# Kernel optimization log

Hardware: AMD Instinct MI355X
Metric: run time of the kernel (lower is better)

The kernel has to match this reference:

```python
import jax, jax.numpy as jnp
import numpy as np

N, F_IN, H, HEADS, C, E = 4096, 768, 512, 4, 32, 131072
DH = H // HEADS


def gcn_conv(x, W, b, src, dst):
    # PyG GCNConv: add self-loops, symmetric normalization, scatter-add aggregation
    h = x @ W                                   # [N, H_out]
    loop = jnp.arange(N)
    s = jnp.concatenate([src, loop])            # sources incl self-loops
    d = jnp.concatenate([dst, loop])            # targets incl self-loops
    deg = jax.ops.segment_sum(jnp.ones_like(d, dtype=h.dtype), d, num_segments=N)
    dinv = jnp.where(deg > 0, jax.lax.rsqrt(deg), 0.0)
    norm = dinv[s] * dinv[d]                    # [E+N]
    msg = h[s] * norm[:, None]                  # gather + scale
    out = jax.ops.segment_sum(msg, d, num_segments=N)  # scatter-add
    return out + b


def mha(x, in_w, in_b, out_w, out_b):
    # torch.nn.MultiheadAttention, batch=1, q=k=v=x, eval (no dropout)
    qkv = x @ in_w.T + in_b                     # [N, 3H]
    q, k, v = jnp.split(qkv, 3, axis=-1)
    q = q.reshape(N, HEADS, DH)
    k = k.reshape(N, HEADS, DH)
    v = v.reshape(N, HEADS, DH)
    scale = 1.0 / jnp.sqrt(jnp.asarray(DH, x.dtype))
    scores = jnp.einsum('nhd,mhd->hnm', q * scale, k)   # [HEADS, N, N]
    attn = jax.nn.softmax(scores, axis=-1)
    o = jnp.einsum('hnm,mhd->nhd', attn, v).reshape(N, H)
    return o @ out_w.T + out_b


def setup_inputs() -> dict:
    key = jax.random.key(0)
    ks = jax.random.split(key, 12)
    f32 = jnp.float32
    return {
        'x': jax.random.normal(ks[0], (N, F_IN), dtype=f32),
        'edge_index': jax.random.randint(ks[1], (2, E), 0, N, dtype=jnp.int64),
        'W1': jax.random.normal(ks[2], (F_IN, H), dtype=f32) * (1.0 / np.sqrt(F_IN)),
        'b1': jnp.zeros((H,), dtype=f32),
        'in_w': jax.random.normal(ks[3], (3 * H, H), dtype=f32) * (1.0 / np.sqrt(H)),
        'in_b': jnp.zeros((3 * H,), dtype=f32),
        'out_w': jax.random.normal(ks[4], (H, H), dtype=f32) * (1.0 / np.sqrt(H)),
        'out_b': jnp.zeros((H,), dtype=f32),
        'W2': jax.random.normal(ks[5], (H, H), dtype=f32) * (1.0 / np.sqrt(H)),
        'b2': jnp.zeros((H,), dtype=f32),
        'Wc': jax.random.normal(ks[6], (H, C), dtype=f32) * (1.0 / np.sqrt(H)),
        'bc': jnp.zeros((C,), dtype=f32),
    }


def reference(x, edge_index, W1, b1, in_w, in_b, out_w, out_b, W2, b2, Wc, bc):
    src, dst = edge_index[0], edge_index[1]
    h = jax.nn.relu(gcn_conv(x, W1, b1, src, dst))
    h = h + mha(h, in_w, in_b, out_w, out_b)      # residual; dropout is identity (eval)
    h = jax.nn.relu(gcn_conv(h, W2, b2, src, dst))
    return h @ Wc + bc                             # [N, C]
```

## Files before the change

kernel.cpp:

```cpp
#include <hip/hip_runtime.h>

typedef unsigned short u16;
typedef unsigned int u32;
typedef __attribute__((ext_vector_type(8))) short bf16x8;
typedef __attribute__((ext_vector_type(4))) short bf16x4;
typedef __attribute__((ext_vector_type(4))) float f32x4;
typedef __attribute__((ext_vector_type(16))) float f32x16;

__device__ __forceinline__ float b2f(u16 b){ u32 u = ((u32)b)<<16; float f; __builtin_memcpy(&f,&u,4); return f; }
__device__ __forceinline__ u16 f2b(float f){ u32 u; __builtin_memcpy(&u,&f,4); u32 r = (u + 0x7fffu + ((u>>16)&1u)) >> 16; return (u16)r; }
__device__ __forceinline__ u32 cvtpk(float lo, float hi){ u32 r; asm("v_cvt_pk_bf16_f32 %0, %1, %2" : "=v"(r) : "v"(lo), "v"(hi)); return r; }
__device__ __forceinline__ void pswap(u32 &a, u32 &b){ asm("v_permlane32_swap_b32 %0, %1" : "+v"(a), "+v"(b)); }
__device__ __forceinline__ void gload16(const u16* g, u16* l){
  __builtin_amdgcn_global_load_lds((const __attribute__((address_space(1))) void*)g,
                                   (__attribute__((address_space(3))) void*)l, 16, 0, 0);
}

__device__ __forceinline__ void conv_body(const float* __restrict__ in, u16* __restrict__ out, int b, int n){
  int i = (b*256 + threadIdx.x)*4;
  if (i + 3 < n){
    float4 v = *(const float4*)(in + i);
    bf16x4 o;
    o[0]=(short)f2b(v.x); o[1]=(short)f2b(v.y); o[2]=(short)f2b(v.z); o[3]=(short)f2b(v.w);
    *(bf16x4*)(out + i) = o;
  } else {
    for (; i<n; ++i) out[i]=f2b(in[i]);
  }
}
__global__ __launch_bounds__(256) void prep_k(const float* __restrict__ x, const float* __restrict__ inw,
    const float* __restrict__ outw, const float* __restrict__ W1, const float* __restrict__ W2,
    const float* __restrict__ Wc, const int* __restrict__ dst, int E,
    u16* __restrict__ Xb, u16* __restrict__ inWb, u16* __restrict__ outWb,
    u16* __restrict__ W1T, u16* __restrict__ W2T, u16* __restrict__ WcT, int* __restrict__ deg){
  __shared__ float tile[32][33];
  int b = blockIdx.x;
  if (b < 3072){ conv_body(x, Xb, b, 4096*768); return; }
  if (b < 3840){ conv_body(inw, inWb, b-3072, 1536*512); return; }
  if (b < 4096){ conv_body(outw, outWb, b-3840, 512*512); return; }
  if (b < 4752){
    const float* in; u16* out; int R, C, bx, by;
    if (b < 4480){ in=W1; out=W1T; R=768; C=512; int lb=b-4096; bx=lb&15; by=lb>>4; }
    else if (b < 4736){ in=W2; out=W2T; R=512; C=512; int lb=b-4480; bx=lb&15; by=lb>>4; }
    else { in=Wc; out=WcT; R=512; C=32; bx=0; by=b-4736; }
    int tx = threadIdx.x & 31, ty = threadIdx.x >> 5;
    int c0 = bx*32, r0 = by*32;
    #pragma unroll
    for (int k=0;k<4;++k){
      int r = r0 + ty + k*8, c = c0 + tx;
      if (r < R && c < C) tile[ty+k*8][tx] = in[(size_t)r*C + c];
    }
    __syncthreads();
    #pragma unroll
    for (int k=0;k<4;++k){
      int c = c0 + ty + k*8, r = r0 + tx;
      if (r < R && c < C) out[(size_t)c*R + r] = f2b(tile[tx][ty+k*8]);
    }
    return;
  }
  int e = (b-4752)*256 + threadIdx.x;
  if (e < E) atomicAdd(&deg[dst[e]], 1);
}

__global__ __launch_bounds__(256) void scan_k(const int* __restrict__ deg, int* __restrict__ row_ptr,
                                              int* __restrict__ cursor, float* __restrict__ dinv){
  __shared__ int lds[256];
  int t = threadIdx.x;
  int base = t*16;
  int cnt[16]; int s = 0;
  #pragma unroll
  for (int k=0;k<16;++k){
    int d = deg[base+k] + 1;
    cnt[k] = d - 1;
    s += d - 1;
    dinv[base+k] = 1.0f / sqrtf((float)d);
  }
  lds[t] = s; __syncthreads();
  for (int o=1;o<256;o<<=1){
    int v = (t>=o) ? lds[t-o] : 0;
    __syncthreads();
    lds[t] += v;
    __syncthreads();
  }
  int run = lds[t] - s;
  #pragma unroll
  for (int k=0;k<16;++k){ row_ptr[base+k] = run; cursor[base+k] = run; run += cnt[k]; }
  if (t == 255) row_ptr[4096] = run;
}
__global__ __launch_bounds__(256) void scatter_k(const int* __restrict__ src, const int* __restrict__ dst,
                                                 int* __restrict__ cursor, int* __restrict__ srcl, int E){
  int e = blockIdx.x*256 + threadIdx.x;
  if (e < E){
    int d = dst[e];
    int pos = atomicAdd(&cursor[d], 1);
    srcl[pos] = src[e];
  }
}

__global__ __launch_bounds__(64) void aggregate_k(const u16* __restrict__ H, const float* __restrict__ dinv,
                                                  const int* __restrict__ rp, const int* __restrict__ srcl,
                                                  const float* __restrict__ bias, u16* __restrict__ out){
  const int i = blockIdx.x, t = threadIdx.x;
  const float di = dinv[i];
  float a[8];
  {
    bf16x8 hv = *(const bf16x8*)(H + (size_t)i*512 + t*8);
    float wself = di*di;
    #pragma unroll
    for (int j=0;j<8;++j) a[j] = b2f((u16)hv[j])*wself;
  }
  int e0 = rp[i], e1 = rp[i+1];
  int e = e0;
  for (; e+3 < e1; e += 4){
    int s0 = srcl[e], s1 = srcl[e+1], s2 = srcl[e+2], s3 = srcl[e+3];
    float w0 = dinv[s0]*di, w1 = dinv[s1]*di, w2 = dinv[s2]*di, w3 = dinv[s3]*di;
    bf16x8 v0 = *(const bf16x8*)(H + (size_t)s0*512 + t*8);
    bf16x8 v1 = *(const bf16x8*)(H + (size_t)s1*512 + t*8);
    bf16x8 v2 = *(const bf16x8*)(H + (size_t)s2*512 + t*8);
    bf16x8 v3 = *(const bf16x8*)(H + (size_t)s3*512 + t*8);
    #pragma unroll
    for (int j=0;j<8;++j){
      a[j] += b2f((u16)v0[j])*w0 + b2f((u16)v1[j])*w1 + b2f((u16)v2[j])*w2 + b2f((u16)v3[j])*w3;
    }
  }
  for (; e < e1; ++e){
    int s = srcl[e];
    float w = dinv[s]*di;
    bf16x8 v = *(const bf16x8*)(H + (size_t)s*512 + t*8);
    #pragma unroll
    for (int j=0;j<8;++j) a[j] += b2f((u16)v[j])*w;
  }
  bf16x8 o;
  #pragma unroll
  for (int j=0;j<8;++j){
    float v = fmaxf(a[j] + bias[t*8+j], 0.f);
    o[j] = (short)f2b(v);
  }
  *(bf16x8*)(out + (size_t)i*512 + t*8) = o;
}

template<int BM,int BN,int WM,int WN,bool BIAS,bool RESID,bool RELU,bool OUTBF,bool QKV>
__global__ __launch_bounds__(256) void gemm_abt_k(
    const u16* __restrict__ A, const u16* __restrict__ B,
    const float* __restrict__ bias, const u16* __restrict__ resid,
    u16* __restrict__ vt, void* __restrict__ Cp, int M, int N, int K)
{
  constexpr int BK = 64;
  constexpr int AISS = (BM*BK)/(256*8);
  constexpr int BISS = (BN*BK)/(256*8);
  constexpr int WC = BN/WN;
  constexpr int FM = WM/16, FN = WN/16;
  constexpr float QS = 0.088388347648318447f * 1.4426950408889634f;
  __shared__ u16 As[BM*BK];
  __shared__ u16 Bs[BN*BK];
  const int tid = threadIdx.x;
  const int wv = tid>>6, ln = tid&63;
  const int l15 = ln&15, l4 = ln>>4;
  const int wm = wv / WC, wn = wv % WC;
  const int bm0 = blockIdx.x*BM, bn0 = blockIdx.y*BN;
  const int arow = tid>>3;
  const int acol = (tid&7)*8;
  f32x4 acc[FM][FN];
  #pragma unroll
  for (int a=0;a<FM;++a)
    #pragma unroll
    for (int b=0;b<FN;++b) acc[a][b] = f32x4{0.f,0.f,0.f,0.f};
  for (int kt=0; kt<K; kt+=BK){
    #pragma unroll
    for (int i=0;i<AISS;++i) gload16(A + (size_t)(bm0 + i*32 + arow)*K + kt + acol, &As[i*2048 + wv*512]);
    #pragma unroll
    for (int i=0;i<BISS;++i) gload16(B + (size_t)(bn0 + i*32 + arow)*K + kt + acol, &Bs[i*2048 + wv*512]);
    __syncthreads();
    #pragma unroll
    for (int kc=0;kc<2;++kc){
      bf16x8 af[FM], bfr[FN];
      #pragma unroll
      for (int a=0;a<FM;++a) af[a] = *(const bf16x8*)(&As[(wm*WM + a*16 + l15)*BK + kc*32 + l4*8]);
      #pragma unroll
      for (int b=0;b<FN;++b) bfr[b] = *(const bf16x8*)(&Bs[(wn*WN + b*16 + l15)*BK + kc*32 + l4*8]);
      #pragma unroll
      for (int a=0;a<FM;++a)
        #pragma unroll
        for (int b=0;b<FN;++b)
          acc[a][b] = __builtin_amdgcn_mfma_f32_16x16x32_bf16(af[a], bfr[b], acc[a][b], 0,0,0);
    }
    __syncthreads();
  }
  #pragma unroll
  for (int a=0;a<FM;++a)
    #pragma unroll
    for (int b=0;b<FN;++b){
      int r0 = bm0 + wm*WM + a*16 + l4*4;
      int c  = bn0 + wn*WN + b*16 + l15;
      if constexpr (QKV){
        float v0 = acc[a][b][0] + bias[c];
        float v1 = acc[a][b][1] + bias[c];
        float v2 = acc[a][b][2] + bias[c];
        float v3 = acc[a][b][3] + bias[c];
        if (c >= 1024){
          bf16x4 pk; pk[0]=(short)f2b(v0); pk[1]=(short)f2b(v1); pk[2]=(short)f2b(v2); pk[3]=(short)f2b(v3);
          *(bf16x4*)(vt + (size_t)(c-1024)*4096 + r0) = pk;
        } else {
          float s = (c < 512) ? QS : 1.0f;
          u16* o = (u16*)Cp;
          o[(size_t)(r0+0)*N + c] = f2b(v0*s);
          o[(size_t)(r0+1)*N + c] = f2b(v1*s);
          o[(size_t)(r0+2)*N + c] = f2b(v2*s);
          o[(size_t)(r0+3)*N + c] = f2b(v3*s);
        }
      } else {
        #pragma unroll
        for (int j=0;j<4;++j){
          int r = r0 + j;
          float v = acc[a][b][j];
          if (BIAS)  v += bias[c];
          if (RESID) v += b2f(resid[(size_t)r*N + c]);
          if (RELU)  v = fmaxf(v, 0.f);
          if (OUTBF) ((u16*)Cp)[(size_t)r*N + c] = f2b(v);
          else       ((float*)Cp)[(size_t)r*N + c] = v;
        }
      }
    }
}

__global__ __launch_bounds__(256,2) void attn_k(const u16* __restrict__ qkv, const u16* __restrict__ vtg,
                                                float* __restrict__ Op, float* __restrict__ Lp){
  __shared__ u16 Ks[64*128];
  __shared__ u16 Vs[128*128];
  const int head = blockIdx.y, split = blockIdx.z;
  const int qb0 = blockIdx.x*128;
  const int tid = threadIdx.x, wv = tid>>6, ln = tid&63;
  const int l31 = ln&31, hi = ln>>5;
  bf16x8 qf[8];
  {
    const u16* qp = qkv + (size_t)(qb0 + wv*32 + l31)*1536 + head*128 + hi*8;
    #pragma unroll
    for (int kk=0;kk<8;++kk) qf[kk] = *(const bf16x8*)(qp + kk*16);
  }
  f32x16 acc_o[4];
  #pragma unroll
  for (int d=0;d<4;++d)
    #pragma unroll
    for (int r=0;r<16;++r) acc_o[d][r] = 0.f;
  float l_part = 0.f;
  const int kR = ln, kG = wv*4;
  const int vR = tid>>1, vG = (tid&1)*4;
  const u16* kbase = qkv + 512 + (size_t)head*128;
  const u16* vbase = vtg + (size_t)(head*128 + vR)*4096;
  const int kv00 = split*1024;
  bf16x8 kreg[4], vreg[4];
  #pragma unroll
  for (int i=0;i<4;++i){
    kreg[i] = *(const bf16x8*)(kbase + (size_t)(kv00 + kR)*1536 + (kG+i)*8);
    vreg[i] = *(const bf16x8*)(vbase + kv00 + (vG+i)*8);
  }
  for (int it=0; it<16; ++it){
    #pragma unroll
    for (int i=0;i<4;++i){
      *(bf16x8*)((char*)Ks + kR*256 + (((kG+i)*16) ^ ((kR&15)<<4))) = kreg[i];
      *(bf16x8*)((char*)Vs + vR*256 + (((vG+i)*16) ^ ((vR&15)<<4))) = vreg[i];
    }
    __syncthreads();
    if (it < 15){
      int nb = kv00 + (it+1)*64;
      #pragma unroll
      for (int i=0;i<4;++i){
        kreg[i] = *(const bf16x8*)(kbase + (size_t)(nb + kR)*1536 + (kG+i)*8);
        vreg[i] = *(const bf16x8*)(vbase + nb + (vG+i)*8);
      }
    }
    f32x16 s0, s1;
    #pragma unroll
    for (int r=0;r<16;++r){ s0[r]=0.f; s1[r]=0.f; }
    #pragma unroll
    for (int kk=0;kk<8;++kk){
      int r0 = l31, r1 = 32 + l31;
      bf16x8 k0 = *(const bf16x8*)((char*)Ks + r0*256 + ((kk*32 + hi*16) ^ ((r0&15)<<4)));
      bf16x8 k1 = *(const bf16x8*)((char*)Ks + r1*256 + ((kk*32 + hi*16) ^ ((r1&15)<<4)));
      s0 = __builtin_amdgcn_mfma_f32_32x32x16_bf16(k0, qf[kk], s0, 0,0,0);
      s1 = __builtin_amdgcn_mfma_f32_32x32x16_bf16(k1, qf[kk], s1, 0,0,0);
    }
    union PU { u32 w[4]; bf16x8 v; };
    PU pa[4];
    #pragma unroll
    for (int g=0; g<2; ++g){
      float p[16];
      #pragma unroll
      for (int r=0;r<16;++r){ float sv = g ? s1[r] : s0[r]; p[r] = __builtin_amdgcn_exp2f(sv); l_part += p[r]; }
      u32 c0=cvtpk(p[0],p[1]), c1=cvtpk(p[2],p[3]), c2=cvtpk(p[4],p[5]), c3=cvtpk(p[6],p[7]);
      u32 c4=cvtpk(p[8],p[9]), c5=cvtpk(p[10],p[11]), c6=cvtpk(p[12],p[13]), c7=cvtpk(p[14],p[15]);
      pswap(c0,c2); pswap(c1,c3); pswap(c4,c6); pswap(c5,c7);
      pa[g*2+0].w[0]=c0; pa[g*2+0].w[1]=c1; pa[g*2+0].w[2]=c2; pa[g*2+0].w[3]=c3;
      pa[g*2+1].w[0]=c4; pa[g*2+1].w[1]=c5; pa[g*2+1].w[2]=c6; pa[g*2+1].w[3]=c7;
    }
    #pragma unroll
    for (int dg=0;dg<4;++dg){
      int row = dg*32 + l31;
      #pragma unroll
      for (int kvf=0;kvf<4;++kvf){
        bf16x8 vf = *(const bf16x8*)((char*)Vs + row*256 + ((kvf*32 + hi*16) ^ ((row&15)<<4)));
        acc_o[dg] = __builtin_amdgcn_mfma_f32_32x32x16_bf16(pa[kvf].v, vf, acc_o[dg], 0,0,0);
      }
    }
    __syncthreads();
  }
  float l_tot = l_part + __shfl_xor(l_part, 32, 64);
  if (hi == 0) Lp[split*4096 + qb0 + wv*32 + l31] = l_tot;
  #pragma unroll
  for (int dg=0;dg<4;++dg){
    #pragma unroll
    for (int r=0;r<16;++r){
      int q = qb0 + wv*32 + (r&3) + ((r>>2)<<3) + hi*4;
      Op[((size_t)split*4096 + q)*512 + head*128 + dg*32 + l31] = acc_o[dg][r];
    }
  }
}

__global__ __launch_bounds__(256) void combine_k(const float* __restrict__ Op, const float* __restrict__ Lp,
                                                 u16* __restrict__ oatt){
  int idx = blockIdx.x*256 + threadIdx.x;
  int n = idx >> 6, c8 = (idx & 63) << 3;
  float l = Lp[n] + Lp[4096+n] + Lp[8192+n] + Lp[12288+n];
  float inv = 1.0f/l;
  float acc[8] = {0,0,0,0,0,0,0,0};
  #pragma unroll
  for (int s=0;s<4;++s){
    const float* p = Op + ((size_t)(s*4096+n))*512 + c8;
    float4 u = *(const float4*)p;
    float4 v = *(const float4*)(p+4);
    acc[0]+=u.x; acc[1]+=u.y; acc[2]+=u.z; acc[3]+=u.w;
    acc[4]+=v.x; acc[5]+=v.y; acc[6]+=v.z; acc[7]+=v.w;
  }
  bf16x8 o;
  #pragma unroll
  for (int j=0;j<8;++j) o[j] = (short)f2b(acc[j]*inv);
  *(bf16x8*)(oatt + (size_t)n*512 + c8) = o;
}

extern "C" void kernel_launch(void* const* d_in, const int* in_sizes, int n_in,
                              void* d_out, int out_size, void* d_ws, size_t ws_size,
                              hipStream_t stream) {
  (void)n_in; (void)out_size; (void)ws_size;
  const float* x    = (const float*)d_in[0];
  const int*   ei   = (const int*)d_in[1];
  const float* W1   = (const float*)d_in[2];
  const float* b1   = (const float*)d_in[3];
  const float* inw  = (const float*)d_in[4];
  const float* inb  = (const float*)d_in[5];
  const float* outw = (const float*)d_in[6];
  const float* outb = (const float*)d_in[7];
  const float* W2   = (const float*)d_in[8];
  const float* b2   = (const float*)d_in[9];
  const float* Wc   = (const float*)d_in[10];
  const float* bc   = (const float*)d_in[11];
  float* out = (float*)d_out;
  const int E = in_sizes[1] / 2;
  const int* srcp = ei;
  const int* dstp = ei + E;

  char* base = (char*)d_ws;
  size_t off = 0;
  auto alloc = [&](size_t bytes)->void*{
    void* p = base + off;
    off = (off + bytes + 255) & ~((size_t)255);
    return p;
  };
  u16* Xb    = (u16*)alloc((size_t)4096*768*2);
  u16* W1T   = (u16*)alloc((size_t)512*768*2);
  u16* inWb  = (u16*)alloc((size_t)1536*512*2);
  u16* outWb = (u16*)alloc((size_t)512*512*2);
  u16* W2T   = (u16*)alloc((size_t)512*512*2);
  u16* WcT   = (u16*)alloc((size_t)32*512*2);
  u16* Hpre  = (u16*)alloc((size_t)4096*512*2);
  u16* h1    = (u16*)alloc((size_t)4096*512*2);
  u16* qkvb  = (u16*)alloc((size_t)4096*1536*2);
  u16* vtg   = (u16*)alloc((size_t)512*4096*2);
  u16* oatt  = (u16*)alloc((size_t)4096*512*2);
  u16* h2    = (u16*)alloc((size_t)4096*512*2);
  u16* h3    = (u16*)alloc((size_t)4096*512*2);
  float* Opart = (float*)alloc((size_t)4*4096*512*4);
  float* Lpart = (float*)alloc((size_t)4*4096*4);
  int*   deg  = (int*)alloc(4096*4);
  float* dinv = (float*)alloc(4096*4);
  int*   rowp = (int*)alloc(4097*4);
  int*   curs = (int*)alloc(4096*4);
  int*   srcl = (int*)alloc((size_t)E*4);

  hipMemsetAsync(deg, 0, 4096*sizeof(int), stream);
  int degBlocks = (E + 255)/256;
  prep_k<<<4752 + degBlocks, 256, 0, stream>>>(x, inw, outw, W1, W2, Wc, dstp, E,
                                               Xb, inWb, outWb, W1T, W2T, WcT, deg);
  scan_k<<<1,256,0,stream>>>(deg, rowp, curs, dinv);
  scatter_k<<<(E+255)/256,256,0,stream>>>(srcp, dstp, curs, srcl, E);

  gemm_abt_k<64,64,32,32,false,false,false,true,false><<<dim3(64,8),256,0,stream>>>(Xb, W1T, nullptr, nullptr, nullptr, Hpre, 4096, 512, 768);
  aggregate_k<<<4096,64,0,stream>>>(Hpre, dinv, rowp, srcl, b1, h1);

  gemm_abt_k<64,128,32,64,true,false,false,true,true><<<dim3(64,12),256,0,stream>>>(h1, inWb, inb, nullptr, vtg, qkvb, 4096, 1536, 512);
  attn_k<<<dim3(32,4,4),256,0,stream>>>(qkvb, vtg, Opart, Lpart);
  combine_k<<<1024,256,0,stream>>>(Opart, Lpart, oatt);
  gemm_abt_k<64,64,32,32,true,true,false,true,false><<<dim3(64,8),256,0,stream>>>(oatt, outWb, outb, h1, nullptr, h2, 4096, 512, 512);

  gemm_abt_k<64,64,32,32,false,false,false,true,false><<<dim3(64,8),256,0,stream>>>(h2, W2T, nullptr, nullptr, nullptr, Hpre, 4096, 512, 512);
  aggregate_k<<<4096,64,0,stream>>>(Hpre, dinv, rowp, srcl, b2, h3);

  gemm_abt_k<64,32,16,32,true,false,false,false,false><<<dim3(64,1),256,0,stream>>>(h3, WcT, bc, nullptr, nullptr, out, 4096, 32, 512);
}
```

Before: 166.8 us.

## Process 64 queries per wave in attention to double K/V tile reuse

Each wave in the attention kernel now handles two 32-row query blocks (64 queries) instead of one, so every K and V tile loaded into shared memory serves twice as many queries. The grid is halved along the query dimension to match. This cuts global-to-LDS traffic and synchronisation per unit of work, at the cost of doubled accumulator and Q-fragment registers. The occupancy hint in launch bounds is dropped, and with half as many blocks (256 total) on a large GPU, occupancy and parallelism may fall.

Result: no change. 166.5 us (-0.2%).

```diff
diff --git a/kernel.cpp b/kernel.cpp
--- a/kernel.cpp
+++ b/kernel.cpp
@@ -222,26 +222,26 @@
     }
 }
 
-__global__ __launch_bounds__(256,2) void attn_k(const u16* __restrict__ qkv, const u16* __restrict__ vtg,
-                                                float* __restrict__ Op, float* __restrict__ Lp){
+__global__ __launch_bounds__(256) void attn_k(const u16* __restrict__ qkv, const u16* __restrict__ vtg,
+                                              float* __restrict__ Op, float* __restrict__ Lp){
   __shared__ u16 Ks[64*128];
   __shared__ u16 Vs[128*128];
   const int head = blockIdx.y, split = blockIdx.z;
-  const int qb0 = blockIdx.x*128;
+  const int qbase = blockIdx.x*256 + (threadIdx.x>>6)*64;
   const int tid = threadIdx.x, wv = tid>>6, ln = tid&63;
   const int l31 = ln&31, hi = ln>>5;
-  bf16x8 qf[8];
+  bf16x8 qfA[8], qfB[8];
   {
-    const u16* qp = qkv + (size_t)(qb0 + wv*32 + l31)*1536 + head*128 + hi*8;
-    #pragma unroll
-    for (int kk=0;kk<8;++kk) qf[kk] = *(const bf16x8*)(qp + kk*16);
-  }
-  f32x16 acc_o[4];
+    const u16* qp = qkv + (size_t)(qbase + l31)*1536 + head*128 + hi*8;
+    #pragma unroll
+    for (int kk=0;kk<8;++kk){ qfA[kk] = *(const bf16x8*)(qp + kk*16); qfB[kk] = *(const bf16x8*)(qp + 32*1536 + kk*16); }
+  }
+  f32x16 accA[4], accB[4];
   #pragma unroll
   for (int d=0;d<4;++d)
     #pragma unroll
-    for (int r=0;r<16;++r) acc_o[d][r] = 0.f;
-  float l_part = 0.f;
+    for (int r=0;r<16;++r){ accA[d][r] = 0.f; accB[d][r] = 0.f; }
+  float lA = 0.f, lB = 0.f;
   const int kR = ln, kG = wv*4;
   const int vR = tid>>1, vG = (tid&1)*4;
   const u16* kbase = qkv + 512 + (size_t)head*128;
@@ -253,6 +253,7 @@
     kreg[i] = *(const bf16x8*)(kbase + (size_t)(kv00 + kR)*1536 + (kG+i)*8);
     vreg[i] = *(const bf16x8*)(vbase + kv00 + (vG+i)*8);
   }
+  union PU { u32 w[4]; bf16x8 v; };
   for (int it=0; it<16; ++it){
     #pragma unroll
     for (int i=0;i<4;++i){
@@ -268,29 +269,54 @@
         vreg[i] = *(const bf16x8*)(vbase + nb + (vG+i)*8);
       }
     }
-    f32x16 s0, s1;
-    #pragma unroll
-    for (int r=0;r<16;++r){ s0[r]=0.f; s1[r]=0.f; }
-    #pragma unroll
-    for (int kk=0;kk<8;++kk){
-      int r0 = l31, r1 = 32 + l31;
-      bf16x8 k0 = *(const bf16x8*)((char*)Ks + r0*256 + ((kk*32 + hi*16) ^ ((r0&15)<<4)));
-      bf16x8 k1 = *(const bf16x8*)((char*)Ks + r1*256 + ((kk*32 + hi*16) ^ ((r1&15)<<4)));
-      s0 = __builtin_amdgcn_mfma_f32_32x32x16_bf16(k0, qf[kk], s0, 0,0,0);
-      s1 = __builtin_amdgcn_mfma_f32_32x32x16_bf16(k1, qf[kk], s1, 0,0,0);
-    }
-    union PU { u32 w[4]; bf16x8 v; };
-    PU pa[4];
-    #pragma unroll
-    for (int g=0; g<2; ++g){
-      float p[16];
-      #pragma unroll
-      for (int r=0;r<16;++r){ float sv = g ? s1[r] : s0[r]; p[r] = __builtin_amdgcn_exp2f(sv); l_part += p[r]; }
-      u32 c0=cvtpk(p[0],p[1]), c1=cvtpk(p[2],p[3]), c2=cvtpk(p[4],p[5]), c3=cvtpk(p[6],p[7]);
-      u32 c4=cvtpk(p[8],p[9]), c5=cvtpk(p[10],p[11]), c6=cvtpk(p[12],p[13]), c7=cvtpk(p[14],p[15]);
-      pswap(c0,c2); pswap(c1,c3); pswap(c4,c6); pswap(c5,c7);
-      pa[g*2+0].w[0]=c0; pa[g*2+0].w[1]=c1; pa[g*2+0].w[2]=c2; pa[g*2+0].w[3]=c3;
-      pa[g*2+1].w[0]=c4; pa[g*2+1].w[1]=c5; pa[g*2+1].w[2]=c6; pa[g*2+1].w[3]=c7;
+    PU paA[4], paB[4];
+    {
+      f32x16 s0, s1;
+      #pragma unroll
+      for (int r=0;r<16;++r){ s0[r]=0.f; s1[r]=0.f; }
+      #pragma unroll
+      for (int kk=0;kk<8;++kk){
+        int r0 = l31, r1 = 32 + l31;
+        bf16x8 k0 = *(const bf16x8*)((char*)Ks + r0*256 + ((kk*32 + hi*16) ^ ((r0&15)<<4)));
+        bf16x8 k1 = *(const bf16x8*)((char*)Ks + r1*256 + ((kk*32 + hi*16) ^ ((r1&15)<<4)));
+        s0 = __builtin_amdgcn_mfma_f32_32x32x16_bf16(k0, qfA[kk], s0, 0,0,0);
+        s1 = __builtin_amdgcn_mfma_f32_32x32x16_bf16(k1, qfA[kk], s1, 0,0,0);
+      }
+      #pragma unroll
+      for (int g=0; g<2; ++g){
+        float p[16];
+        #pragma unroll
+        for (int r=0;r<16;++r){ float sv = g ? s1[r] : s0[r]; p[r] = __builtin_amdgcn_exp2f(sv); lA += p[r]; }
+        u32 c0=cvtpk(p[0],p[1]), c1=cvtpk(p[2],p[3]), c2=cvtpk(p[4],p[5]), c3=cvtpk(p[6],p[7]);
+        u32 c4=cvtpk(p[8],p[9]), c5=cvtpk(p[10],p[11]), c6=cvtpk(p[12],p[13]), c7=cvtpk(p[14],p[15]);
+        pswap(c0,c2); pswap(c1,c3); pswap(c4,c6); pswap(c5,c7);
+        paA[g*2+0].w[0]=c0; paA[g*2+0].w[1]=c1; paA[g*2+0].w[2]=c2; paA[g*2+0].w[3]=c3;
+        paA[g*2+1].w[0]=c4; paA[g*2+1].w[1]=c5; paA[g*2+1].w[2]=c6; paA[g*2+1].w[3]=c7;
+      }
+    }
+    {
+      f32x16 s0, s1;
+      #pragma unroll
+      for (int r=0;r<16;++r){ s0[r]=0.f; s1[r]=0.f; }
+      #pragma unroll
+      for (int kk=0;kk<8;++kk){
+        int r0 = l31, r1 = 32 + l31;
+        bf16x8 k0 = *(const bf16x8*)((char*)Ks + r0*256 + ((kk*32 + hi*16) ^ ((r0&15)<<4)));
+        bf16x8 k1 = *(const bf16x8*)((char*)Ks + r1*256 + ((kk*32 + hi*16) ^ ((r1&15)<<4)));
+        s0 = __builtin_amdgcn_mfma_f32_32x32x16_bf16(k0, qfB[kk], s0, 0,0,0);
+        s1 = __builtin_amdgcn_mfma_f32_32x32x16_bf16(k1, qfB[kk], s1, 0,0,0);
+      }
+      #pragma unroll
+      for (int g=0; g<2; ++g){
+        float p[16];
+        #pragma unroll
+        for (int r=0;r<16;++r){ float sv = g ? s1[r] : s0[r]; p[r] = __builtin_amdgcn_exp2f(sv); lB += p[r]; }
+        u32 c0=cvtpk(p[0],p[1]), c1=cvtpk(p[2],p[3]), c2=cvtpk(p[4],p[5]), c3=cvtpk(p[6],p[7]);
+        u32 c4=cvtpk(p[8],p[9]), c5=cvtpk(p[10],p[11]), c6=cvtpk(p[12],p[13]), c7=cvtpk(p[14],p[15]);
+        pswap(c0,c2); pswap(c1,c3); pswap(c4,c6); pswap(c5,c7);
+        paB[g*2+0].w[0]=c0; paB[g*2+0].w[1]=c1; paB[g*2+0].w[2]=c2; paB[g*2+0].w[3]=c3;
+        paB[g*2+1].w[0]=c4; paB[g*2+1].w[1]=c5; paB[g*2+1].w[2]=c6; paB[g*2+1].w[3]=c7;
+      }
     }
     #pragma unroll
     for (int dg=0;dg<4;++dg){
@@ -298,19 +324,25 @@
       #pragma unroll
       for (int kvf=0;kvf<4;++kvf){
         bf16x8 vf = *(const bf16x8*)((char*)Vs + row*256 + ((kvf*32 + hi*16) ^ ((row&15)<<4)));
-        acc_o[dg] = __builtin_amdgcn_mfma_f32_32x32x16_bf16(pa[kvf].v, vf, acc_o[dg], 0,0,0);
-      }
-    }
-    __syncthreads();
-  }
-  float l_tot = l_part + __shfl_xor(l_part, 32, 64);
-  if (hi == 0) Lp[split*4096 + qb0 + wv*32 + l31] = l_tot;
+        accA[dg] = __builtin_amdgcn_mfma_f32_32x32x16_bf16(paA[kvf].v, vf, accA[dg], 0,0,0);
+        accB[dg] = __builtin_amdgcn_mfma_f32_32x32x16_bf16(paB[kvf].v, vf, accB[dg], 0,0,0);
+      }
+    }
+    __syncthreads();
+  }
+  float ltA = lA + __shfl_xor(lA, 32, 64);
+  float ltB = lB + __shfl_xor(lB, 32, 64);
+  if (hi == 0){
+    Lp[split*4096 + qbase + l31] = ltA;
+    Lp[split*4096 + qbase + 32 + l31] = ltB;
+  }
   #pragma unroll
   for (int dg=0;dg<4;++dg){
     #pragma unroll
     for (int r=0;r<16;++r){
-      int q = qb0 + wv*32 + (r&3) + ((r>>2)<<3) + hi*4;
-      Op[((size_t)split*4096 + q)*512 + head*128 + dg*32 + l31] = acc_o[dg][r];
+      int qo = (r&3) + ((r>>2)<<3) + hi*4;
+      Op[((size_t)split*4096 + qbase + qo)*512 + head*128 + dg*32 + l31] = accA[dg][r];
+      Op[((size_t)split*4096 + qbase + 32 + qo)*512 + head*128 + dg*32 + l31] = accB[dg][r];
     }
   }
 }
@@ -396,7 +428,7 @@
   aggregate_k<<<4096,64,0,stream>>>(Hpre, dinv, rowp, srcl, b1, h1);
 
   gemm_abt_k<64,128,32,64,true,false,false,true,true><<<dim3(64,12),256,0,stream>>>(h1, inWb, inb, nullptr, vtg, qkvb, 4096, 1536, 512);
-  attn_k<<<dim3(32,4,4),256,0,stream>>>(qkvb, vtg, Opart, Lpart);
+  attn_k<<<dim3(16,4,4),256,0,stream>>>(qkvb, vtg, Opart, Lpart);
   combine_k<<<1024,256,0,stream>>>(Opart, Lpart, oatt);
   gemm_abt_k<64,64,32,32,true,true,false,true,false><<<dim3(64,8),256,0,stream>>>(oatt, outWb, outb, h1, nullptr, h2, 4096, 512, 512);
 
```
